# Kernel optimization log

Measured on AMD Instinct MI355X. Metric: run time of the kernel, lower is better.

## Reference

```python
import jax, jax.numpy as jnp
import numpy as np
import math

B, C, L, N, HEAD, M, DEPTH = 16, 256, 64, 8192, 8, 12, 1
PI = math.pi
MODES = jnp.arange(M, dtype=jnp.float32) / M  # modes_list = i/num_basis


def conv1d(x, w, b=None):
    # 1x1 Conv1d == channel matmul. x: (B,Cin,T), w: (Cout,Cin)
    y = jnp.einsum('oc,bcn->bon', w, x)
    if b is not None:
        y = y + b[None, :, None]
    return y


def split_heads(x):
    # (B,C,T) -> (B,H,T,c)  matching view(B,head,C//head,T).permute(0,1,3,2)
    b, c, t = x.shape
    return x.reshape(b, HEAD, c // HEAD, t).transpose(0, 1, 3, 2)


def merge_heads(x):
    # (B,H,T,c) -> (B,C,T)
    b, h, t, c = x.shape
    return x.transpose(0, 1, 3, 2).reshape(b, h * c, t)


def self_attn(q, k, v):
    # NOTE: source multiplies by dim**0.5 (not 1/sqrt(dim)); keep faithful.
    dim = q.shape[-1]
    a = jax.nn.softmax(jnp.einsum('bhlc,bhsc->bhls', q, k) * (dim ** 0.5), axis=-1)
    return jnp.einsum('bhls,bhsc->bhlc', a, v)


def encoder(x, enc_w, enc_b, weights):
    b, c, l = x.shape
    qkv = conv1d(x, enc_w, enc_b).reshape(b, 3, c, l)
    q = split_heads(qkv[:, 0])
    k = split_heads(qkv[:, 1])
    v = split_heads(qkv[:, 2])
    attn = merge_heads(self_attn(q, k, v))  # (B,C,L)
    # Fourier basis: cat(sin, cos) over num_basis modes -> (B,C,L,2M)
    ph = MODES[None, None, None, :] * attn[..., None] * PI
    basis = jnp.concatenate([jnp.sin(ph), jnp.cos(ph)], axis=-1)
    return jnp.einsum('bclm,cm->bcl', basis, weights) + x


def decoder(x, attn, dec_w, dec_b):
    kv = split_heads(attn)                      # (B,H,L,c) latent keys/values
    q = split_heads(conv1d(x, dec_w, dec_b))    # (B,H,N,c) point queries
    return merge_heads(self_attn(q, kv, kv)) + x


def bn_lrelu(x, g, b):
    # eval-mode BatchNorm1d (running_mean=0, running_var=1, eps=1e-5) + LeakyReLU(0.2)
    y = g[None, :, None] * x / jnp.sqrt(1.0 + 1e-5) + b[None, :, None]
    return jnp.where(y >= 0, y, 0.2 * y)


def setup_inputs() -> dict:
    key = jax.random.key(0)
    ks = jax.random.split(key, 8)
    return {
        'xt': jax.random.normal(ks[0], (B, C, L), jnp.float32),
        'xn': jax.random.normal(ks[1], (B, C, N), jnp.float32),
        'weights': jax.random.uniform(ks[2], (C, 2 * M), jnp.float32) / C,
        'mask_token': jax.random.normal(ks[3], (1, C, 1), jnp.float32) * 0.02,
        'enc_w': jax.random.normal(ks[4], (3 * C, C), jnp.float32) * 0.02,
        'enc_b': jnp.zeros((3 * C,), jnp.float32),
        'dec_w': jax.random.normal(ks[5], (C, C), jnp.float32) * 0.02,
        'dec_b': jnp.zeros((C,), jnp.float32),
        'fc1_w': jax.random.normal(ks[6], (C, C), jnp.float32) * 0.02,
        'fc1_g': jnp.ones((C,), jnp.float32),
        'fc1_b': jnp.zeros((C,), jnp.float32),
        'fc2_w': jax.random.normal(ks[7], (3, C), jnp.float32) * 0.02,
        'fc2_g': jnp.ones((3,), jnp.float32),
        'fc2_b': jnp.zeros((3,), jnp.float32),
    }


def reference(xt, xn, weights, mask_token, enc_w, enc_b, dec_w, dec_b,
              fc1_w, fc1_g, fc1_b, fc2_w, fc2_g, fc2_b):
    b = xt.shape[0]
    n = xn.shape[-1]
    # ratio=1.0 -> len_keep=0 -> fully masked: mask_token broadcast, under no_grad
    x_masked = jax.lax.stop_gradient(jnp.broadcast_to(mask_token, (b, C, n)))
    enc = xt
    x = x_masked
    for _ in range(DEPTH):
        enc = encoder(enc, enc_w, enc_b, weights)
        x = decoder(x, enc, dec_w, dec_b)
    xn_pre = x
    y = bn_lrelu(conv1d(xn_pre, fc1_w), fc1_g, fc1_b)
    y = bn_lrelu(conv1d(y, fc2_w), fc2_g, fc2_b)  # (B,3,N)
    return xn_pre, y.transpose(0, 2, 1)  # ((B,C,N), (B,N,3))
```

## Files before the change

### kernel.cpp

```cpp
#include <hip/hip_runtime.h>
#include <hip/hip_bf16.h>
#include <math.h>

#define B_    16
#define C_    256
#define L_    64
#define N_    8192
#define HEAD_ 8
#define HC_   32
#define M_    12

#define SQRT32F 5.656854249492380f
#define PI_F    3.14159265358979323846f
#define BN_INV  0.99999500003749969f

typedef float v4f __attribute__((ext_vector_type(4)));

__global__ __launch_bounds__(512) void fused_enc(
    const float* __restrict__ xt, const float* __restrict__ enc_w,
    const float* __restrict__ enc_b, const float* __restrict__ weights,
    const float* __restrict__ dec_w, const float* __restrict__ dec_b,
    const float* __restrict__ mt, float* __restrict__ xnp_out)
{
    __shared__ float Xs[C_][L_];
    __shared__ float qkv_s[96][68];
    __shared__ float P[L_][68];
    __shared__ float enc_t[HC_][68];
    __shared__ float qvs[HC_];
    __shared__ float aw[L_];
    const int t = threadIdx.x;
    const int b = blockIdx.x >> 3;
    const int h = blockIdx.x & 7;
    const float* xtb = xt + (size_t)b * (C_ * L_);

    #pragma unroll
    for (int i = 0; i < 8; ++i) {
        int q = t + i * 512;
        int c = q >> 4, l4 = (q & 15) * 4;
        *reinterpret_cast<float4*>(&Xs[c][l4]) =
            *reinterpret_cast<const float4*>(&xtb[q * 4]);
    }
    __syncthreads();

    {
        const int tx = t & 15, ty = t >> 4;
        float acc[3][4] = {};
        int og[3];
        const float* wrow[3];
        #pragma unroll
        for (int r = 0; r < 3; ++r) {
            int o_loc = ty * 3 + r;
            int sec = o_loc >> 5, cc = o_loc & 31;
            og[r] = sec * C_ + h * HC_ + cc;
            wrow[r] = enc_w + (size_t)og[r] * C_;
        }
        #pragma unroll 2
        for (int c0 = 0; c0 < C_; c0 += 4) {
            float4 x0 = *reinterpret_cast<const float4*>(&Xs[c0 + 0][tx * 4]);
            float4 x1 = *reinterpret_cast<const float4*>(&Xs[c0 + 1][tx * 4]);
            float4 x2 = *reinterpret_cast<const float4*>(&Xs[c0 + 2][tx * 4]);
            float4 x3 = *reinterpret_cast<const float4*>(&Xs[c0 + 3][tx * 4]);
            #pragma unroll
            for (int r = 0; r < 3; ++r) {
                float4 w4 = *reinterpret_cast<const float4*>(&wrow[r][c0]);
                acc[r][0] += w4.x * x0.x + w4.y * x1.x + w4.z * x2.x + w4.w * x3.x;
                acc[r][1] += w4.x * x0.y + w4.y * x1.y + w4.z * x2.y + w4.w * x3.y;
                acc[r][2] += w4.x * x0.z + w4.y * x1.z + w4.z * x2.z + w4.w * x3.z;
                acc[r][3] += w4.x * x0.w + w4.y * x1.w + w4.z * x2.w + w4.w * x3.w;
            }
        }
        #pragma unroll
        for (int r = 0; r < 3; ++r) {
            float bias = enc_b[og[r]];
            float4 v = make_float4(acc[r][0] + bias, acc[r][1] + bias,
                                   acc[r][2] + bias, acc[r][3] + bias);
            *reinterpret_cast<float4*>(&qkv_s[ty * 3 + r][tx * 4]) = v;
        }
    }
    if (t < 128) {
        int cc = t >> 2, part = t & 3;
        const float* wr = dec_w + (size_t)(h * HC_ + cc) * C_ + part * 64;
        const float* mp = mt + part * 64;
        float s = 0.f;
        #pragma unroll
        for (int j = 0; j < 16; ++j) {
            float4 w4 = *reinterpret_cast<const float4*>(&wr[j * 4]);
            float4 m4 = *reinterpret_cast<const float4*>(&mp[j * 4]);
            s += w4.x * m4.x + w4.y * m4.y + w4.z * m4.z + w4.w * m4.w;
        }
        s += __shfl_xor(s, 1);
        s += __shfl_xor(s, 2);
        if (part == 0) qvs[cc] = s + dec_b[h * HC_ + cc];
    }
    __syncthreads();

    #pragma unroll
    for (int i = 0; i < 2; ++i) {
        int q = t + i * 512;
        int l = q >> 4, lq = (q & 15) * 4;
        float4 a4 = make_float4(0.f, 0.f, 0.f, 0.f);
        #pragma unroll
        for (int cc = 0; cc < HC_; ++cc) {
            float qv_ = qkv_s[cc][l];
            float4 k4 = *reinterpret_cast<const float4*>(&qkv_s[32 + cc][lq]);
            a4.x += qv_ * k4.x; a4.y += qv_ * k4.y;
            a4.z += qv_ * k4.z; a4.w += qv_ * k4.w;
        }
        a4.x *= SQRT32F; a4.y *= SQRT32F; a4.z *= SQRT32F; a4.w *= SQRT32F;
        *reinterpret_cast<float4*>(&P[l][lq]) = a4;
    }
    __syncthreads();

    if (t < 256) {
        int l = t >> 2, p0 = (t & 3) * 16;
        float m = -1e30f;
        #pragma unroll
        for (int j = 0; j < 16; ++j) m = fmaxf(m, P[l][p0 + j]);
        m = fmaxf(m, __shfl_xor(m, 1));
        m = fmaxf(m, __shfl_xor(m, 2));
        float sum = 0.f;
        #pragma unroll
        for (int j = 0; j < 16; ++j) {
            float e = __expf(P[l][p0 + j] - m);
            P[l][p0 + j] = e;
            sum += e;
        }
        sum += __shfl_xor(sum, 1);
        sum += __shfl_xor(sum, 2);
        float inv = 1.0f / sum;
        #pragma unroll
        for (int j = 0; j < 16; ++j) P[l][p0 + j] *= inv;
    }
    __syncthreads();

    #pragma unroll
    for (int i = 0; i < 4; ++i) {
        int e  = t + i * 512;
        int cc = e >> 6, l = e & 63;
        float a = 0.f;
        #pragma unroll
        for (int sq = 0; sq < 16; ++sq) {
            float4 p4 = *reinterpret_cast<const float4*>(&P[l][sq * 4]);
            float4 v4 = *reinterpret_cast<const float4*>(&qkv_s[64 + cc][sq * 4]);
            a += p4.x * v4.x + p4.y * v4.y + p4.z * v4.z + p4.w * v4.w;
        }
        int c = h * HC_ + cc;
        float val = Xs[c][l];
        const float* wr = weights + c * (2 * M_);
        float base = a * (PI_F / (float)M_);
        #pragma unroll
        for (int m = 0; m < M_; ++m) {
            float sn, cs;
            __sincosf((float)m * base, &sn, &cs);
            val += wr[m] * sn + wr[M_ + m] * cs;
        }
        enc_t[cc][l] = val;
    }
    __syncthreads();

    if (t < L_) {
        float s = 0.f;
        #pragma unroll
        for (int cc = 0; cc < HC_; ++cc) s += qvs[cc] * enc_t[cc][t];
        s *= SQRT32F;
        float m = s;
        #pragma unroll
        for (int off = 32; off >= 1; off >>= 1) m = fmaxf(m, __shfl_xor(m, off));
        float e = __expf(s - m);
        float sum = e;
        #pragma unroll
        for (int off = 32; off >= 1; off >>= 1) sum += __shfl_xor(sum, off);
        aw[t] = e / sum;
    }
    __syncthreads();
    if (t < HC_) {
        float a = 0.f;
        #pragma unroll
        for (int k4 = 0; k4 < L_; k4 += 4) {
            float4 a4 = *reinterpret_cast<const float4*>(&aw[k4]);
            float4 v4 = *reinterpret_cast<const float4*>(&enc_t[t][k4]);
            a += a4.x * v4.x + a4.y * v4.y + a4.z * v4.z + a4.w * v4.w;
        }
        int c = h * HC_ + t;
        xnp_out[b * C_ + c] = a + mt[c];
    }
}

__global__ __launch_bounds__(256) void bcast_fc(const float* __restrict__ xnp,
                                                const float* __restrict__ fc1_w,
                                                const float* __restrict__ fc1_g,
                                                const float* __restrict__ fc1_b,
                                                const float* __restrict__ fc2_w,
                                                const float* __restrict__ fc2_g,
                                                const float* __restrict__ fc2_b,
                                                float* __restrict__ out) {
    const int t = threadIdx.x;
    const int blk = blockIdx.x;
    if (blk >= 16) {
        int rowid = blk - 16;
        float v = xnp[rowid];
        v4f V = {v, v, v, v};
        v4f* row = reinterpret_cast<v4f*>(out + (size_t)rowid * N_);
        #pragma unroll
        for (int i = 0; i < 8; ++i)
            __builtin_nontemporal_store(V, &row[t + i * 256]);
    } else {
        int b = blk;
        __shared__ float xs[C_];
        __shared__ float y1[C_];
        __shared__ float y2s[4];
        xs[t] = xnp[b * C_ + t];
        __syncthreads();
        {
            const float* wrow = fc1_w + (size_t)t * C_;
            float s = 0.f;
            #pragma unroll 8
            for (int c4 = 0; c4 < C_; c4 += 4) {
                float4 w4 = *reinterpret_cast<const float4*>(&wrow[c4]);
                float4 x4 = *reinterpret_cast<const float4*>(&xs[c4]);
                s += w4.x * x4.x + w4.y * x4.y + w4.z * x4.z + w4.w * x4.w;
            }
            float y = fc1_g[t] * s * BN_INV + fc1_b[t];
            y1[t] = (y >= 0.f) ? y : 0.2f * y;
        }
        __syncthreads();
        if (t < 3) {
            const float* wrow = fc2_w + t * C_;
            float s = 0.f;
            #pragma unroll 8
            for (int c4 = 0; c4 < C_; c4 += 4) {
                float4 w4 = *reinterpret_cast<const float4*>(&wrow[c4]);
                float4 x4 = *reinterpret_cast<const float4*>(&y1[c4]);
                s += w4.x * x4.x + w4.y * x4.y + w4.z * x4.z + w4.w * x4.w;
            }
            float y = fc2_g[t] * s * BN_INV + fc2_b[t];
            y2s[t] = (y >= 0.f) ? y : 0.2f * y;
        }
        __syncthreads();
        float v0 = y2s[0], v1 = y2s[1], v2 = y2s[2];
        v4f pat0 = {v0, v1, v2, v0};
        v4f pat1 = {v1, v2, v0, v1};
        v4f pat2 = {v2, v0, v1, v2};
        int r = t % 3;
        v4f a = (r == 0) ? pat0 : (r == 1) ? pat1 : pat2;
        v4f bb = (r == 0) ? pat1 : (r == 1) ? pat2 : pat0;
        v4f c = (r == 0) ? pat2 : (r == 1) ? pat0 : pat1;
        v4f* o1 = reinterpret_cast<v4f*>(
            out + (size_t)B_ * C_ * N_ + (size_t)b * (N_ * 3));
        #pragma unroll
        for (int i = 0; i < 24; i += 3) {
            __builtin_nontemporal_store(a,  &o1[t + (i + 0) * 256]);
            __builtin_nontemporal_store(bb, &o1[t + (i + 1) * 256]);
            __builtin_nontemporal_store(c,  &o1[t + (i + 2) * 256]);
        }
    }
}

extern "C" void kernel_launch(void* const* d_in, const int* in_sizes, int n_in,
                              void* d_out, int out_size, void* d_ws, size_t ws_size,
                              hipStream_t stream) {
    const float* xt      = (const float*)d_in[0];
    const float* weights = (const float*)d_in[2];
    const float* mt      = (const float*)d_in[3];
    const float* enc_w   = (const float*)d_in[4];
    const float* enc_b   = (const float*)d_in[5];
    const float* dec_w   = (const float*)d_in[6];
    const float* dec_b   = (const float*)d_in[7];
    const float* fc1_w   = (const float*)d_in[8];
    const float* fc1_g   = (const float*)d_in[9];
    const float* fc1_b   = (const float*)d_in[10];
    const float* fc2_w   = (const float*)d_in[11];
    const float* fc2_g   = (const float*)d_in[12];
    const float* fc2_b   = (const float*)d_in[13];

    float* ws  = (float*)d_ws;
    float* xnp = ws;

    float* out = (float*)d_out;

    fused_enc<<<128, 512, 0, stream>>>(xt, enc_w, enc_b, weights,
                                       dec_w, dec_b, mt, xnp);
    bcast_fc<<<4112, 256, 0, stream>>>(xnp, fc1_w, fc1_g, fc1_b,
                                       fc2_w, fc2_g, fc2_b, out);
}
```

Baseline: 59.13 us.

## Stage QKV projection weights through double-buffered LDS tiles with register prefetch

The encoder QKV projection now copies 96x32 tiles of enc_w into a double-buffered shared-memory array and prefetches the next tile into registers while computing on the current one. Previously each thread read weight rows straight from global memory inside the inner loop. The decoder query projection of the mask token is also moved earlier so it overlaps the initial loads. In exchange the kernel uses more LDS and adds a barrier per K chunk, which could reduce occupancy.

```diff
diff --git a/kernel.cpp b/kernel.cpp
--- a/kernel.cpp
+++ b/kernel.cpp
@@ -23,6 +23,7 @@
     const float* __restrict__ mt, float* __restrict__ xnp_out)
 {
     __shared__ float Xs[C_][L_];
+    __shared__ float Ws[2][96][36];
     __shared__ float qkv_s[96][68];
     __shared__ float P[L_][68];
     __shared__ float enc_t[HC_][68];
@@ -33,6 +34,11 @@
     const int h = blockIdx.x & 7;
     const float* xtb = xt + (size_t)b * (C_ * L_);
 
+    const int r0  = t >> 3,        c40 = (t & 7) * 4;
+    const int r1  = (512 + t) >> 3, c41 = ((512 + t) & 7) * 4;
+    const size_t og0 = (size_t)((r0 >> 5) * C_ + h * HC_ + (r0 & 31)) * C_;
+    const size_t og1 = (size_t)((r1 >> 5) * C_ + h * HC_ + (r1 & 31)) * C_;
+
     #pragma unroll
     for (int i = 0; i < 8; ++i) {
         int q = t + i * 512;
@@ -40,54 +46,75 @@
         *reinterpret_cast<float4*>(&Xs[c][l4]) =
             *reinterpret_cast<const float4*>(&xtb[q * 4]);
     }
+    {
+        *reinterpret_cast<float4*>(&Ws[0][r0][c40]) =
+            *reinterpret_cast<const float4*>(&enc_w[og0 + c40]);
+        if (t < 256)
+            *reinterpret_cast<float4*>(&Ws[0][r1][c41]) =
+                *reinterpret_cast<const float4*>(&enc_w[og1 + c41]);
+    }
+    float qv_part = 0.f;
+    if (t < 128) {
+        int cc = t >> 2, part = t & 3;
+        const float* wrq = dec_w + (size_t)(h * HC_ + cc) * C_ + part * 64;
+        const float* mp = mt + part * 64;
+        #pragma unroll
+        for (int j = 0; j < 16; ++j) {
+            float4 w4 = *reinterpret_cast<const float4*>(&wrq[j * 4]);
+            float4 m4 = *reinterpret_cast<const float4*>(&mp[j * 4]);
+            qv_part += w4.x * m4.x + w4.y * m4.y + w4.z * m4.z + w4.w * m4.w;
+        }
+    }
     __syncthreads();
 
     {
         const int tx = t & 15, ty = t >> 4;
         float acc[3][4] = {};
-        int og[3];
-        const float* wrow[3];
+        for (int kc = 0; kc < 8; ++kc) {
+            const int buf = kc & 1;
+            float4 pf0, pf1;
+            if (kc < 7) {
+                const size_t k1 = (size_t)(kc + 1) * 32;
+                pf0 = *reinterpret_cast<const float4*>(&enc_w[og0 + k1 + c40]);
+                if (t < 256)
+                    pf1 = *reinterpret_cast<const float4*>(&enc_w[og1 + k1 + c41]);
+            }
+            const int cbase = kc * 32;
+            #pragma unroll
+            for (int kk = 0; kk < 32; kk += 4) {
+                float4 x0 = *reinterpret_cast<const float4*>(&Xs[cbase + kk + 0][tx * 4]);
+                float4 x1 = *reinterpret_cast<const float4*>(&Xs[cbase + kk + 1][tx * 4]);
+                float4 x2 = *reinterpret_cast<const float4*>(&Xs[cbase + kk + 2][tx * 4]);
+                float4 x3 = *reinterpret_cast<const float4*>(&Xs[cbase + kk + 3][tx * 4]);
+                #pragma unroll
+                for (int r = 0; r < 3; ++r) {
+                    float4 w4 = *reinterpret_cast<const float4*>(&Ws[buf][ty * 3 + r][kk]);
+                    acc[r][0] += w4.x * x0.x + w4.y * x1.x + w4.z * x2.x + w4.w * x3.x;
+                    acc[r][1] += w4.x * x0.y + w4.y * x1.y + w4.z * x2.y + w4.w * x3.y;
+                    acc[r][2] += w4.x * x0.z + w4.y * x1.z + w4.z * x2.z + w4.w * x3.z;
+                    acc[r][3] += w4.x * x0.w + w4.y * x1.w + w4.z * x2.w + w4.w * x3.w;
+                }
+            }
+            if (kc < 7) {
+                *reinterpret_cast<float4*>(&Ws[buf ^ 1][r0][c40]) = pf0;
+                if (t < 256)
+                    *reinterpret_cast<float4*>(&Ws[buf ^ 1][r1][c41]) = pf1;
+                __syncthreads();
+            }
+        }
         #pragma unroll
         for (int r = 0; r < 3; ++r) {
             int o_loc = ty * 3 + r;
-            int sec = o_loc >> 5, cc = o_loc & 31;
-            og[r] = sec * C_ + h * HC_ + cc;
-            wrow[r] = enc_w + (size_t)og[r] * C_;
-        }
-        #pragma unroll 2
-        for (int c0 = 0; c0 < C_; c0 += 4) {
-            float4 x0 = *reinterpret_cast<const float4*>(&Xs[c0 + 0][tx * 4]);
-            float4 x1 = *reinterpret_cast<const float4*>(&Xs[c0 + 1][tx * 4]);
-            float4 x2 = *reinterpret_cast<const float4*>(&Xs[c0 + 2][tx * 4]);
-            float4 x3 = *reinterpret_cast<const float4*>(&Xs[c0 + 3][tx * 4]);
-            #pragma unroll
-            for (int r = 0; r < 3; ++r) {
-                float4 w4 = *reinterpret_cast<const float4*>(&wrow[r][c0]);
-                acc[r][0] += w4.x * x0.x + w4.y * x1.x + w4.z * x2.x + w4.w * x3.x;
-                acc[r][1] += w4.x * x0.y + w4.y * x1.y + w4.z * x2.y + w4.w * x3.y;
-                acc[r][2] += w4.x * x0.z + w4.y * x1.z + w4.z * x2.z + w4.w * x3.z;
-                acc[r][3] += w4.x * x0.w + w4.y * x1.w + w4.z * x2.w + w4.w * x3.w;
-            }
-        }
-        #pragma unroll
-        for (int r = 0; r < 3; ++r) {
-            float bias = enc_b[og[r]];
+            int og = (o_loc >> 5) * C_ + h * HC_ + (o_loc & 31);
+            float bias = enc_b[og];
             float4 v = make_float4(acc[r][0] + bias, acc[r][1] + bias,
                                    acc[r][2] + bias, acc[r][3] + bias);
-            *reinterpret_cast<float4*>(&qkv_s[ty * 3 + r][tx * 4]) = v;
+            *reinterpret_cast<float4*>(&qkv_s[o_loc][tx * 4]) = v;
         }
     }
     if (t < 128) {
         int cc = t >> 2, part = t & 3;
-        const float* wr = dec_w + (size_t)(h * HC_ + cc) * C_ + part * 64;
-        const float* mp = mt + part * 64;
-        float s = 0.f;
-        #pragma unroll
-        for (int j = 0; j < 16; ++j) {
-            float4 w4 = *reinterpret_cast<const float4*>(&wr[j * 4]);
-            float4 m4 = *reinterpret_cast<const float4*>(&mp[j * 4]);
-            s += w4.x * m4.x + w4.y * m4.y + w4.z * m4.z + w4.w * m4.w;
-        }
+        float s = qv_part;
         s += __shfl_xor(s, 1);
         s += __shfl_xor(s, 2);
         if (part == 0) qvs[cc] = s + dec_b[h * HC_ + cc];
```

Result: slower. 63.14 us (+6.8%).

## Register-tile encoder attention matmuls, stage Fourier weights in LDS, use sincos recurrence

Applied to the files above, without the earlier changes.

The QK^T and PV products in the encoder block now use register tiles of 4x4 and 4x2 per thread on 256 threads instead of one output per thread, which cuts the number of LDS loads per FMA. The per-channel Fourier weights are staged into shared memory. The 12 sincos calls per element are replaced by one sincos followed by an angle-addition recurrence. In exchange, half the threads sit idle in these phases, and the recurrence can accumulate rounding error.

```diff
diff --git a/kernel.cpp b/kernel.cpp
--- a/kernel.cpp
+++ b/kernel.cpp
@@ -26,6 +26,7 @@
     __shared__ float qkv_s[96][68];
     __shared__ float P[L_][68];
     __shared__ float enc_t[HC_][68];
+    __shared__ float wts[HC_][24];
     __shared__ float qvs[HC_];
     __shared__ float aw[L_];
     const int t = threadIdx.x;
@@ -40,6 +41,9 @@
         *reinterpret_cast<float4*>(&Xs[c][l4]) =
             *reinterpret_cast<const float4*>(&xtb[q * 4]);
     }
+    #pragma unroll
+    for (int idx = t; idx < HC_ * 24; idx += 512)
+        wts[idx / 24][idx % 24] = weights[(h * HC_) * 24 + idx];
     __syncthreads();
 
     {
@@ -94,20 +98,27 @@
     }
     __syncthreads();
 
-    #pragma unroll
-    for (int i = 0; i < 2; ++i) {
-        int q = t + i * 512;
-        int l = q >> 4, lq = (q & 15) * 4;
-        float4 a4 = make_float4(0.f, 0.f, 0.f, 0.f);
+    if (t < 256) {
+        const int l0  = (t >> 4) * 4;
+        const int lp0 = (t & 15) * 4;
+        float sc[4][4] = {};
         #pragma unroll
         for (int cc = 0; cc < HC_; ++cc) {
-            float qv_ = qkv_s[cc][l];
-            float4 k4 = *reinterpret_cast<const float4*>(&qkv_s[32 + cc][lq]);
-            a4.x += qv_ * k4.x; a4.y += qv_ * k4.y;
-            a4.z += qv_ * k4.z; a4.w += qv_ * k4.w;
-        }
-        a4.x *= SQRT32F; a4.y *= SQRT32F; a4.z *= SQRT32F; a4.w *= SQRT32F;
-        *reinterpret_cast<float4*>(&P[l][lq]) = a4;
+            float4 q4 = *reinterpret_cast<const float4*>(&qkv_s[cc][l0]);
+            float4 k4 = *reinterpret_cast<const float4*>(&qkv_s[32 + cc][lp0]);
+            float qs[4] = {q4.x, q4.y, q4.z, q4.w};
+            #pragma unroll
+            for (int i = 0; i < 4; ++i) {
+                sc[i][0] += qs[i] * k4.x; sc[i][1] += qs[i] * k4.y;
+                sc[i][2] += qs[i] * k4.z; sc[i][3] += qs[i] * k4.w;
+            }
+        }
+        #pragma unroll
+        for (int i = 0; i < 4; ++i) {
+            float4 v = make_float4(sc[i][0] * SQRT32F, sc[i][1] * SQRT32F,
+                                   sc[i][2] * SQRT32F, sc[i][3] * SQRT32F);
+            *reinterpret_cast<float4*>(&P[l0 + i][lp0]) = v;
+        }
     }
     __syncthreads();
 
@@ -133,28 +144,51 @@
     }
     __syncthreads();
 
-    #pragma unroll
-    for (int i = 0; i < 4; ++i) {
-        int e  = t + i * 512;
-        int cc = e >> 6, l = e & 63;
-        float a = 0.f;
+    if (t < 256) {
+        const int l0 = (t >> 4) * 4;
+        const int c0 = (t & 15) * 2;
+        float a[4][2] = {};
         #pragma unroll
         for (int sq = 0; sq < 16; ++sq) {
-            float4 p4 = *reinterpret_cast<const float4*>(&P[l][sq * 4]);
-            float4 v4 = *reinterpret_cast<const float4*>(&qkv_s[64 + cc][sq * 4]);
-            a += p4.x * v4.x + p4.y * v4.y + p4.z * v4.z + p4.w * v4.w;
-        }
-        int c = h * HC_ + cc;
-        float val = Xs[c][l];
-        const float* wr = weights + c * (2 * M_);
-        float base = a * (PI_F / (float)M_);
-        #pragma unroll
-        for (int m = 0; m < M_; ++m) {
-            float sn, cs;
-            __sincosf((float)m * base, &sn, &cs);
-            val += wr[m] * sn + wr[M_ + m] * cs;
-        }
-        enc_t[cc][l] = val;
+            float4 p4[4], v4[2];
+            #pragma unroll
+            for (int i = 0; i < 4; ++i)
+                p4[i] = *reinterpret_cast<const float4*>(&P[l0 + i][sq * 4]);
+            #pragma unroll
+            for (int j = 0; j < 2; ++j)
+                v4[j] = *reinterpret_cast<const float4*>(&qkv_s[64 + c0 + j][sq * 4]);
+            #pragma unroll
+            for (int i = 0; i < 4; ++i)
+                #pragma unroll
+                for (int j = 0; j < 2; ++j)
+                    a[i][j] += p4[i].x * v4[j].x + p4[i].y * v4[j].y
+                             + p4[i].z * v4[j].z + p4[i].w * v4[j].w;
+        }
+        #pragma unroll
+        for (int j = 0; j < 2; ++j) {
+            int cc = c0 + j;
+            int c  = h * HC_ + cc;
+            const float* wrf = wts[cc];
+            float vv[4];
+            #pragma unroll
+            for (int i = 0; i < 4; ++i) {
+                float val = Xs[c][l0 + i] + wrf[M_];
+                float base = a[i][j] * (PI_F / (float)M_);
+                float s1, c1;
+                __sincosf(base, &s1, &c1);
+                float sm = 0.f, cm = 1.f;
+                #pragma unroll
+                for (int m = 1; m < M_; ++m) {
+                    float sp = sm * c1 + cm * s1;
+                    float cp = cm * c1 - sm * s1;
+                    sm = sp; cm = cp;
+                    val += wrf[m] * sm + wrf[M_ + m] * cm;
+                }
+                vv[i] = val;
+            }
+            *reinterpret_cast<float4*>(&enc_t[cc][l0]) =
+                make_float4(vv[0], vv[1], vv[2], vv[3]);
+        }
     }
     __syncthreads();
 
```

After: 54.44 us. 7.9% less time.
